# Performance work log

Measured on AMD Instinct MI355X. Metric: run time of the kernel, lower is better.

## Reference

```python
import jax, jax.numpy as jnp
import numpy as np

DIM_H = 384
EPS = 0.5
HID = 768
NN = 3   # num_normal_labels (B,I,O)
NL = 7   # num_labels (O, B/I x POS/NEG/NEU)


def _make_w_trans():
    # ote_vocab: B=0, I=1, O=2 ; ts_vocab: O=0, B-POS=1, B-NEG=2, B-NEU=3, I-POS=4, I-NEG=5, I-NEU=6
    W = np.zeros((NN, NL), dtype=np.float32)
    W[0, 1] = W[0, 2] = W[0, 3] = 1.0 / 3.0  # B -> B-*
    W[1, 4] = W[1, 5] = W[1, 6] = 1.0 / 3.0  # I -> I-*
    W[2, 0] = 1.0                            # O -> O
    return jnp.asarray(W)


def setup_inputs() -> dict:
    key = jax.random.key(0)
    ks = jax.random.split(key, 16)
    B, S = 32, 512
    s = 0.02
    inp = {
        'x': jax.random.normal(ks[0], (B, S, HID), jnp.float32),
        'attention_mask': jnp.ones((B, S), jnp.int32),
        'labels': jax.random.randint(ks[1], (B, S), 0, NL, jnp.int32),
        'labels_normal': jax.random.randint(ks[2], (B, S), 0, NN, jnp.int32),
        'W_fc_normal': jax.random.normal(ks[3], (HID, NN), jnp.float32) * s,
        'b_fc_normal': jnp.zeros((NN,), jnp.float32),
        'w_ih_f': jax.random.normal(ks[4], (4 * DIM_H, HID), jnp.float32) * s,
        'w_hh_f': jax.random.normal(ks[5], (4 * DIM_H, DIM_H), jnp.float32) * s,
        'b_f': jnp.zeros((4 * DIM_H,), jnp.float32),
        'w_ih_b': jax.random.normal(ks[6], (4 * DIM_H, HID), jnp.float32) * s,
        'w_hh_b': jax.random.normal(ks[7], (4 * DIM_H, DIM_H), jnp.float32) * s,
        'b_b': jnp.zeros((4 * DIM_H,), jnp.float32),
        'W_gate': jax.random.uniform(ks[8], (2 * DIM_H, 2 * DIM_H), jnp.float32, -0.2, 0.2),
        'W_fc_upper': jax.random.normal(ks[9], (2 * DIM_H, NL), jnp.float32) * s,
        'b_fc_upper': jnp.zeros((NL,), jnp.float32),
        'W_trans': _make_w_trans(),
    }
    return inp


def _lstm_dir(xs, w_ih, w_hh, b):
    # xs: [S, B, HID] time-major; PyTorch gate order i,f,g,o
    B = xs.shape[1]
    pre = jnp.einsum('sbh,gh->sbg', xs, w_ih) + b  # precompute input projections

    def step(carry, p_t):
        h, c = carry
        g = p_t + h @ w_hh.T
        i, f, gg, o = jnp.split(g, 4, axis=-1)
        c = jax.nn.sigmoid(f) * c + jax.nn.sigmoid(i) * jnp.tanh(gg)
        h = jax.nn.sigmoid(o) * jnp.tanh(c)
        return (h, c), h

    init = (jnp.zeros((B, DIM_H), xs.dtype), jnp.zeros((B, DIM_H), xs.dtype))
    _, hs = jax.lax.scan(step, init, pre)
    return hs  # [S, B, DIM_H]


def _masked_ce(logits, labels, mask):
    logp = jax.nn.log_softmax(logits, axis=-1)
    nll = -jnp.take_along_axis(logp, labels[..., None].astype(jnp.int32), axis=-1)[..., 0]
    m = mask.astype(logits.dtype)
    return jnp.sum(nll * m) / jnp.sum(m)


def reference(x, attention_mask, labels, labels_normal, W_fc_normal, b_fc_normal,
              w_ih_f, w_hh_f, b_f, w_ih_b, w_hh_b, b_b, W_gate,
              W_fc_upper, b_fc_upper, W_trans):
    z_t = x @ W_fc_normal + b_fc_normal                      # [B,S,NN]
    loss = _masked_ce(z_t, labels_normal, attention_mask)

    xs = jnp.transpose(x, (1, 0, 2))                         # [S,B,HID]
    hf = _lstm_dir(xs, w_ih_f, w_hh_f, b_f)
    hb = _lstm_dir(xs[::-1], w_ih_b, w_hh_b, b_b)[::-1]
    h_s = jnp.concatenate([hf, hb], axis=-1)                 # [S,B,2*DIM_H]

    # gated highway recurrence: gates depend only on h_s -> batched matmul + linear scan
    g = jax.nn.sigmoid(h_s @ W_gate)                         # [S,B,768]

    def gate_step(h_prev, inp):
        ht, gt = inp
        h = gt * ht + (1.0 - gt) * h_prev
        return h, h

    _, rest = jax.lax.scan(gate_step, h_s[0], (h_s[1:], g[1:]))
    h_tilde = jnp.concatenate([h_s[:1], rest], axis=0)       # [S,B,768]
    h_tilde = jnp.transpose(h_tilde, (1, 0, 2))              # [B,S,768]; dropout = identity (eval)

    z_s = h_tilde @ W_fc_upper + b_fc_upper                  # [B,S,NL]
    p = jax.nn.softmax(z_t, axis=-1)
    alpha = EPS * jnp.sum(p * p, axis=-1, keepdims=True)     # [B,S,1]
    z_s_prime = z_t @ W_trans                                # [B,S,NL]
    z_s_tilde = z_s_prime * alpha + z_s * (1.0 - alpha)

    loss = loss + _masked_ce(z_s_tilde, labels, attention_mask)
    return loss, z_s_tilde
```

## Files before the change

kernel.cpp:

```cpp
#include <hip/hip_runtime.h>

#define B_SZ   32
#define S_LEN  512
#define HID    768
#define DH     384
#define G4     1536
#define NPOS   16384
#define EPS_C  0.5f
#define NCH    24576
#define CHK    64
#define NCHK   8

typedef _Float16 h2 __attribute__((ext_vector_type(2)));
typedef short bf16x8 __attribute__((ext_vector_type(8)));
typedef float f32x4 __attribute__((ext_vector_type(4)));

static __device__ __forceinline__ float sigm(float x) { return 1.0f / (1.0f + __expf(-x)); }
static __device__ __forceinline__ float tanh_fast(float x) {
    return 1.0f - 2.0f / (__expf(2.0f * x) + 1.0f);
}

static __device__ __forceinline__ unsigned short f2bf(float f) {
    union { float f; unsigned u; } v; v.f = f;
    unsigned r = v.u + 0x7FFF + ((v.u >> 16) & 1);
    return (unsigned short)(r >> 16);
}
static __device__ __forceinline__ float bf2f(unsigned short u) {
    union { unsigned u; float f; } v; v.u = ((unsigned)u) << 16; return v.f;
}

static __device__ __forceinline__ float wred(float v) {
#pragma unroll
    for (int off = 32; off > 0; off >>= 1) v += __shfl_down(v, off, 64);
    return v;
}

static __device__ __forceinline__ float dot2acc(h2 a, h2 b, float c) {
#if __has_builtin(__builtin_amdgcn_fdot2)
    return __builtin_amdgcn_fdot2(a, b, c, false);
#else
    return c + (float)a.x * (float)b.x + (float)a.y * (float)b.y;
#endif
}

__global__ void wprep(const float* __restrict__ wf, const float* __restrict__ wb,
                      unsigned* __restrict__ wpk) {
    int gid = blockIdx.x * 256 + threadIdx.x;
    int d = (gid >= 294912) ? 1 : 0;
    int j = gid - d * 294912;
    const float* src = d ? wb : wf;
    _Float16 a = (_Float16)src[2 * j];
    _Float16 b = (_Float16)src[2 * j + 1];
    unsigned pa = __builtin_bit_cast(unsigned short, a);
    unsigned pb = __builtin_bit_cast(unsigned short, b);
    wpk[(size_t)d * 294912 + j] = pa | (pb << 16);
}

__global__ __launch_bounds__(256) void cast_bf16(
    const float* __restrict__ src, unsigned short* __restrict__ dst, int n4) {
    int i = blockIdx.x * 256 + threadIdx.x;
    if (i >= n4) return;
    float4 v = *(const float4*)(src + (size_t)i * 4);
    ushort4 o;
    o.x = f2bf(v.x); o.y = f2bf(v.y); o.z = f2bf(v.z); o.w = f2bf(v.w);
    *(ushort4*)(dst + (size_t)i * 4) = o;
}

__global__ __launch_bounds__(256) void wgt_prep(
    const float* __restrict__ Wg, unsigned short* __restrict__ Wgt) {
    int i = blockIdx.x * 256 + threadIdx.x;
    int k = i / 768, n = i - k * 768;
    Wgt[(size_t)n * 768 + k] = f2bf(Wg[i]);
}

__global__ __launch_bounds__(256) void zt_kernel(
    const float* __restrict__ x, const int* __restrict__ amask,
    const int* __restrict__ labn, const float* __restrict__ Wfc,
    const float* __restrict__ bfc, const float* __restrict__ Wtr,
    float* __restrict__ alpha, float* __restrict__ zsp,
    float* __restrict__ p0, float* __restrict__ p2) {
    const int gid  = blockIdx.x * blockDim.x + threadIdx.x;
    const int pos  = gid >> 6, lane = gid & 63, wv = threadIdx.x >> 6;
    __shared__ float r0[4], r2[4];
    const float* xp = x + (size_t)pos * HID;
    float a0 = 0.f, a1 = 0.f, a2 = 0.f;
#pragma unroll
    for (int j = 0; j < 12; ++j) {
        int k = lane + (j << 6);
        float xv = xp[k];
        a0 += xv * Wfc[k * 3 + 0];
        a1 += xv * Wfc[k * 3 + 1];
        a2 += xv * Wfc[k * 3 + 2];
    }
    a0 = wred(a0); a1 = wred(a1); a2 = wred(a2);
    if (lane == 0) {
        float z0 = a0 + bfc[0], z1 = a1 + bfc[1], z2 = a2 + bfc[2];
        float mx = fmaxf(z0, fmaxf(z1, z2));
        float e0 = __expf(z0 - mx), e1 = __expf(z1 - mx), e2 = __expf(z2 - mx);
        float se = e0 + e1 + e2;
        float m  = (float)amask[pos];
        int  lab = labn[pos];
        float zl = (lab == 0) ? z0 : ((lab == 1) ? z1 : z2);
        r0[wv] = (mx + __logf(se) - zl) * m;
        r2[wv] = m;
        float q0 = e0 / se, q1 = e1 / se, q2 = e2 / se;
        alpha[pos] = EPS_C * (q0 * q0 + q1 * q1 + q2 * q2);
#pragma unroll
        for (int cc = 0; cc < 7; ++cc)
            zsp[(size_t)pos * 7 + cc] = z0 * Wtr[cc] + z1 * Wtr[7 + cc] + z2 * Wtr[14 + cc];
    }
    __syncthreads();
    if (threadIdx.x == 0) {
        p0[blockIdx.x] = r0[0] + r0[1] + r0[2] + r0[3];
        p2[blockIdx.x] = r2[0] + r2[1] + r2[2] + r2[3];
    }
}

__global__ __launch_bounds__(256) void gemm_mfma(
    const unsigned short* __restrict__ A, const unsigned short* __restrict__ B,
    const float* __restrict__ bias, void* __restrict__ Cout,
    int M, int N, int K, int mode) {
    __shared__ __align__(16) unsigned short As[128][40];
    __shared__ __align__(16) unsigned short Bs[128][40];
    const int tid = threadIdx.x;
    const int m0 = blockIdx.y * 128, n0 = blockIdx.x * 128;
    const int wave = tid >> 6, lane = tid & 63;
    const int wm = (wave & 1) * 64, wn = (wave >> 1) * 64;
    const int lm = lane & 15, quad = lane >> 4;
    f32x4 acc[4][4] = {};

    for (int k0 = 0; k0 < K; k0 += 32) {
#pragma unroll
        for (int r = 0; r < 2; ++r) {
            int seg = tid + r * 256;
            int row = seg >> 2, c16 = (seg & 3) << 3;
            uint4 va = *(const uint4*)(A + (size_t)(m0 + row) * K + k0 + c16);
            *(uint4*)&As[row][c16] = va;
            uint4 vb = *(const uint4*)(B + (size_t)(n0 + row) * K + k0 + c16);
            *(uint4*)&Bs[row][c16] = vb;
        }
        __syncthreads();
        bf16x8 af[4], bfr[4];
#pragma unroll
        for (int i = 0; i < 4; ++i) {
            af[i]  = *(const bf16x8*)&As[wm + i * 16 + lm][quad * 8];
            bfr[i] = *(const bf16x8*)&Bs[wn + i * 16 + lm][quad * 8];
        }
#pragma unroll
        for (int mi = 0; mi < 4; ++mi)
#pragma unroll
            for (int ni = 0; ni < 4; ++ni)
                acc[mi][ni] = __builtin_amdgcn_mfma_f32_16x16x32_bf16(
                    af[mi], bfr[ni], acc[mi][ni], 0, 0, 0);
        __syncthreads();
    }

    const int rbase = quad * 4;
#pragma unroll
    for (int mi = 0; mi < 4; ++mi) {
#pragma unroll
        for (int ni = 0; ni < 4; ++ni) {
            const int col = n0 + wn + ni * 16 + lm;
            const float bv = (mode == 0) ? bias[col] : 0.0f;
#pragma unroll
            for (int r = 0; r < 4; ++r) {
                const int row = m0 + wm + mi * 16 + rbase + r;
                float v = acc[mi][ni][r];
                if (mode == 0)
                    ((unsigned short*)Cout)[(size_t)row * N + col] = f2bf(v + bv);
                else
                    ((float*)Cout)[(size_t)row * N + col] = sigm(v);
            }
        }
    }
}

#define WLOAD(i) const uint4 wr##i = wq[i];
#define WDOT(i) \
    a0 = dot2acc(__builtin_bit_cast(h2, wr##i.x), hp[4*(i)+0], a0); \
    a1 = dot2acc(__builtin_bit_cast(h2, wr##i.y), hp[4*(i)+1], a1); \
    a2 = dot2acc(__builtin_bit_cast(h2, wr##i.z), hp[4*(i)+2], a2); \
    a3 = dot2acc(__builtin_bit_cast(h2, wr##i.w), hp[4*(i)+3], a3);

__global__ __launch_bounds__(768) void lstm_scan3(
    const unsigned* __restrict__ wpk,
    const unsigned short* __restrict__ pre,
    unsigned short* __restrict__ h_sb,
    unsigned long long* __restrict__ hx64) {
    const int blk   = blockIdx.x;
    const int chain = blk & 63;
    const int bp    = blk >> 6;
    const int d = chain >> 5, b = chain & 31;
    const int tid = threadIdx.x;
    const int r = tid >> 1, p = tid & 1;
    const int g = r / 96;
    const int u = r - g * 96;
    const int base = bp * 96;
    const int G = g * 384 + base + u;

    __shared__ __align__(16) _Float16 lh16[384];
    __shared__ float lpre[384];

    const uint4* wq = (const uint4*)(wpk + ((size_t)d * 1536 + G) * 192 + p * 96);
    WLOAD(0)  WLOAD(1)  WLOAD(2)  WLOAD(3)  WLOAD(4)  WLOAD(5)
    WLOAD(6)  WLOAD(7)  WLOAD(8)  WLOAD(9)  WLOAD(10) WLOAD(11)
    WLOAD(12) WLOAD(13) WLOAD(14) WLOAD(15) WLOAD(16) WLOAD(17)
    WLOAD(18) WLOAD(19) WLOAD(20) WLOAD(21) WLOAD(22) WLOAD(23)

    const unsigned short* prb = pre + ((size_t)d * B_SZ + b) * S_LEN * G4;
    float c = 0.0f;

    for (int s = 0; s < S_LEN; ++s) {
        const int t = d ? (S_LEN - 1 - s) : s;
        float prev = bf2f(prb[(size_t)t * G4 + G]);

        if (s == 0) {
            if (tid < 384) lh16[tid] = (_Float16)0.0f;
        } else if (tid < 288) {
            const int uu = tid + (tid >= base ? 96 : 0);
            const unsigned long long* srcp =
                hx64 + ((size_t)((s - 1) & 1) * 64 + chain) * 384 + uu;
            unsigned long long v =
                __hip_atomic_load(srcp, __ATOMIC_RELAXED, __HIP_MEMORY_SCOPE_AGENT);
            while ((unsigned)(v >> 32) != (unsigned)(s - 1)) {
                __builtin_amdgcn_s_sleep(1);
                v = __hip_atomic_load(srcp, __ATOMIC_RELAXED, __HIP_MEMORY_SCOPE_AGENT);
            }
            lh16[uu] = (_Float16)__builtin_bit_cast(float, (unsigned)v);
        }
        __syncthreads();

        {
            const h2* hp = ((const h2*)lh16) + p * 96;
            float a0 = (p == 0) ? prev : 0.0f, a1 = 0.f, a2 = 0.f, a3 = 0.f;
            WDOT(0)  WDOT(1)  WDOT(2)  WDOT(3)  WDOT(4)  WDOT(5)
            WDOT(6)  WDOT(7)  WDOT(8)  WDOT(9)  WDOT(10) WDOT(11)
            WDOT(12) WDOT(13) WDOT(14) WDOT(15) WDOT(16) WDOT(17)
            WDOT(18) WDOT(19) WDOT(20) WDOT(21) WDOT(22) WDOT(23)
            float acc = (a0 + a1) + (a2 + a3);
            lpre[r] = acc + __shfl_xor(acc, 1, 64);
        }
        __syncthreads();

        if (tid < 96) {
            float gi = lpre[tid], gf = lpre[96 + tid], gg = lpre[192 + tid], go = lpre[288 + tid];
            c = sigm(gf) * c + sigm(gi) * tanh_fast(gg);
            float h = sigm(go) * tanh_fast(c);
            const size_t oidx = ((size_t)t * B_SZ + b) * HID + d * DH + base + tid;
            h_sb[oidx] = f2bf(h);
            lh16[base + tid] = (_Float16)h;
            unsigned long long v = ((unsigned long long)(unsigned)s << 32)
                                 | (unsigned long long)__builtin_bit_cast(unsigned, h);
            __hip_atomic_store(hx64 + ((size_t)(s & 1) * 64 + chain) * 384 + base + tid,
                               v, __ATOMIC_RELAXED, __HIP_MEMORY_SCOPE_AGENT);
        }
    }
}

__global__ __launch_bounds__(256) void gscanA(
    const float* __restrict__ g, const unsigned short* __restrict__ hsb,
    float2* __restrict__ ab) {
    int id = blockIdx.x * 256 + threadIdx.x;
    int chunk = id / NCH, chain = id - chunk * NCH;
    int t0 = chunk * CHK;
    float A = 1.f, Bv = 0.f;
    for (int i = 0; i < CHK; ++i) {
        int t = t0 + i;
        size_t idx = (size_t)t * NCH + chain;
        float gv = g[idx];
        float hv = bf2f(hsb[idx]);
        float a = (t == 0) ? 0.f : (1.f - gv);
        float bb = (t == 0) ? hv : gv * hv;
        A  = a * A;
        Bv = a * Bv + bb;
    }
    ab[id] = make_float2(A, Bv);
}

__global__ __launch_bounds__(256) void gscanB(
    const float2* __restrict__ ab, float* __restrict__ cin) {
    int chain = blockIdx.x * 256 + threadIdx.x;
    float h = 0.f;
#pragma unroll
    for (int j = 0; j < NCHK; ++j) {
        cin[(size_t)j * NCH + chain] = h;
        float2 t = ab[(size_t)j * NCH + chain];
        h = t.x * h + t.y;
    }
}

__global__ __launch_bounds__(256) void gscanC(
    const float* __restrict__ g, const unsigned short* __restrict__ hsb,
    float* __restrict__ hs, const float* __restrict__ cin) {
    int id = blockIdx.x * 256 + threadIdx.x;
    int chunk = id / NCH, chain = id - chunk * NCH;
    int t0 = chunk * CHK;
    float h = cin[(size_t)chunk * NCH + chain];
    for (int i = 0; i < CHK; ++i) {
        int t = t0 + i;
        size_t idx = (size_t)t * NCH + chain;
        float gv = g[idx];
        float v  = bf2f(hsb[idx]);
        h = (t == 0) ? v : (gv * v + (1.f - gv) * h);
        hs[idx] = h;
    }
}

__global__ __launch_bounds__(256) void final_k(
    const float* __restrict__ ht, const float* __restrict__ Wup,
    const float* __restrict__ bup, const float* __restrict__ alpha,
    const float* __restrict__ zsp, const int* __restrict__ labels,
    const int* __restrict__ amask, float* __restrict__ out, float* __restrict__ p1) {
    const int gid = blockIdx.x * blockDim.x + threadIdx.x;
    const int pos = gid >> 6, lane = gid & 63, wv = threadIdx.x >> 6;
    __shared__ float r1[4];
    const int bb = pos >> 9, tt = pos & 511;
    const float* hp = ht + (size_t)tt * (B_SZ * HID) + (size_t)bb * HID;
    float acc[7] = {};
#pragma unroll
    for (int j = 0; j < 12; ++j) {
        int k = lane + (j << 6);
        float hv = hp[k];
        const float* wr = Wup + k * 7;
#pragma unroll
        for (int cc = 0; cc < 7; ++cc) acc[cc] += hv * wr[cc];
    }
#pragma unroll
    for (int cc = 0; cc < 7; ++cc) acc[cc] = wred(acc[cc]);
    if (lane == 0) {
        float al = alpha[pos];
        float z[7], mx = -1e30f;
#pragma unroll
        for (int cc = 0; cc < 7; ++cc) {
            float v = acc[cc] + bup[cc];
            v = zsp[(size_t)pos * 7 + cc] * al + v * (1.0f - al);
            z[cc] = v;
            mx = fmaxf(mx, v);
            out[1 + (size_t)pos * 7 + cc] = v;
        }
        float se = 0.f;
#pragma unroll
        for (int cc = 0; cc < 7; ++cc) se += __expf(z[cc] - mx);
        float lse = mx + __logf(se);
        int lab = labels[pos];
        float zl = z[0];
#pragma unroll
        for (int cc = 1; cc < 7; ++cc) if (lab == cc) zl = z[cc];
        float m = (float)amask[pos];
        r1[wv] = (lse - zl) * m;
    }
    __syncthreads();
    if (threadIdx.x == 0)
        p1[blockIdx.x] = r1[0] + r1[1] + r1[2] + r1[3];
}

__global__ __launch_bounds__(256) void loss_k(
    const float* __restrict__ p0, const float* __restrict__ p1,
    const float* __restrict__ p2, float* __restrict__ out) {
    const int tid = threadIdx.x, lane = tid & 63, wv = tid >> 6;
    __shared__ float rs[4][3];
    float s0 = 0.f, s1 = 0.f, s2 = 0.f;
    for (int i = tid; i < 4096; i += 256) {
        s0 += p0[i]; s1 += p1[i]; s2 += p2[i];
    }
    s0 = wred(s0); s1 = wred(s1); s2 = wred(s2);
    if (lane == 0) { rs[wv][0] = s0; rs[wv][1] = s1; rs[wv][2] = s2; }
    __syncthreads();
    if (tid == 0) {
        float t0 = rs[0][0] + rs[1][0] + rs[2][0] + rs[3][0];
        float t1 = rs[0][1] + rs[1][1] + rs[2][1] + rs[3][1];
        float t2 = rs[0][2] + rs[1][2] + rs[2][2] + rs[3][2];
        out[0] = t0 / t2 + t1 / t2;
    }
}

extern "C" void kernel_launch(void* const* d_in, const int* in_sizes, int n_in,
                              void* d_out, int out_size, void* d_ws, size_t ws_size,
                              hipStream_t stream) {
    const float* x     = (const float*)d_in[0];
    const int*   amask = (const int*)d_in[1];
    const int*   labels= (const int*)d_in[2];
    const int*   labn  = (const int*)d_in[3];
    const float* Wfc   = (const float*)d_in[4];
    const float* bfc   = (const float*)d_in[5];
    const float* wihf  = (const float*)d_in[6];
    const float* whhf  = (const float*)d_in[7];
    const float* bf    = (const float*)d_in[8];
    const float* wihb  = (const float*)d_in[9];
    const float* whhb  = (const float*)d_in[10];
    const float* bb    = (const float*)d_in[11];
    const float* Wg    = (const float*)d_in[12];
    const float* Wup   = (const float*)d_in[13];
    const float* bup   = (const float*)d_in[14];
    const float* Wtr   = (const float*)d_in[15];
    float* out = (float*)d_out;
    (void)in_sizes; (void)n_in; (void)out_size; (void)ws_size;

    char* ws = (char*)d_ws;
    size_t off = 0;
    auto alloc = [&](size_t bytes) -> char* {
        char* p = ws + off;
        off = (off + bytes + 255) & ~(size_t)255;
        return p;
    };
    unsigned* w16buf    = (unsigned*)alloc((size_t)2 * 1536 * 192 * 4);
    unsigned short* pre = (unsigned short*)alloc((size_t)2 * NPOS * G4 * 2);
    float* hs           = (float*)alloc((size_t)NPOS * HID * 4);
    unsigned short* xb  = (unsigned short*)alloc((size_t)NPOS * HID * 2);
    unsigned short* wfb = (unsigned short*)alloc((size_t)G4 * HID * 2);
    unsigned short* wbb = (unsigned short*)alloc((size_t)G4 * HID * 2);
    unsigned short* wgt = (unsigned short*)alloc((size_t)HID * HID * 2);
    float* alpha        = (float*)alloc((size_t)NPOS * 4);
    float* zsp          = (float*)alloc((size_t)NPOS * 7 * 4);
    unsigned long long* hx64 = (unsigned long long*)alloc((size_t)2 * 64 * 384 * 8);
    float2* ab          = (float2*)alloc((size_t)NCHK * NCH * 8);
    float* cin          = (float*)alloc((size_t)NCHK * NCH * 4);
    float* part0        = (float*)alloc(4096 * 4);
    float* part1        = (float*)alloc(4096 * 4);
    float* part2        = (float*)alloc(4096 * 4);
    float* gbuf          = (float*)pre;
    unsigned short* h_sb = xb;


    wprep<<<2304, 256, 0, stream>>>(whhf, whhb, w16buf);
    cast_bf16<<<12288, 256, 0, stream>>>(x, xb, NPOS * HID / 4);
    cast_bf16<<<1152, 256, 0, stream>>>(wihf, wfb, G4 * HID / 4);
    cast_bf16<<<1152, 256, 0, stream>>>(wihb, wbb, G4 * HID / 4);
    wgt_prep<<<2304, 256, 0, stream>>>(Wg, wgt);

    zt_kernel<<<4096, 256, 0, stream>>>(x, amask, labn, Wfc, bfc, Wtr, alpha, zsp,
                                        part0, part2);

    gemm_mfma<<<dim3(12, 128), 256, 0, stream>>>(xb, wfb, bf, pre, NPOS, G4, HID, 0);
    gemm_mfma<<<dim3(12, 128), 256, 0, stream>>>(xb, wbb, bb, pre + (size_t)NPOS * G4,
                                                 NPOS, G4, HID, 0);

    lstm_scan3<<<256, 768, 0, stream>>>(w16buf, pre, h_sb, hx64);

    gemm_mfma<<<dim3(6, 128), 256, 0, stream>>>(h_sb, wgt, nullptr, gbuf, NPOS, HID, HID, 1);

    gscanA<<<768, 256, 0, stream>>>(gbuf, h_sb, ab);
    gscanB<<<96, 256, 0, stream>>>(ab, cin);
    gscanC<<<768, 256, 0, stream>>>(gbuf, h_sb, hs, cin);

    final_k<<<4096, 256, 0, stream>>>(hs, Wup, bup, alpha, zsp, labels, amask, out, part1);

    loss_k<<<1, 256, 0, stream>>>(part0, part1, part2, out);
}
```

Before: 1.291 ms.

## Remap LSTM threads so gate nonlinearity uses shuffles, dropping a block barrier

Threads are remapped so that the eight lanes covering one hidden unit (4 gates x 2 halves) sit together in a wavefront. The i/f/g/o gate sums are then gathered with warp shuffles instead of going through shared memory with a second __syncthreads. The hidden-state buffer in LDS is double-buffered so the new h can be written without racing readers. This removes one block-wide barrier per timestep of the serial recurrence. In exchange, 96 lanes spread across all waves now do the nonlinearity instead of one contiguous group, and a min-blocks-per-CU hint of 3 is added to the launch bounds.

Result: slower. 1.472 ms (+14.0%).

```diff
diff --git a/kernel.cpp b/kernel.cpp
--- a/kernel.cpp
+++ b/kernel.cpp
@@ -182,7 +182,7 @@
     a2 = dot2acc(__builtin_bit_cast(h2, wr##i.z), hp[4*(i)+2], a2); \
     a3 = dot2acc(__builtin_bit_cast(h2, wr##i.w), hp[4*(i)+3], a3);
 
-__global__ __launch_bounds__(768) void lstm_scan3(
+__global__ __launch_bounds__(768, 3) void lstm_scan4(
     const unsigned* __restrict__ wpk,
     const unsigned short* __restrict__ pre,
     unsigned short* __restrict__ h_sb,
@@ -192,14 +192,15 @@
     const int bp    = blk >> 6;
     const int d = chain >> 5, b = chain & 31;
     const int tid = threadIdx.x;
-    const int r = tid >> 1, p = tid & 1;
-    const int g = r / 96;
-    const int u = r - g * 96;
+    const int lane = tid & 63;
+    const int unit = tid >> 3;
+    const int sub  = tid & 7;
+    const int gate = sub >> 1;
+    const int p    = sub & 1;
     const int base = bp * 96;
-    const int G = g * 384 + base + u;
-
-    __shared__ __align__(16) _Float16 lh16[384];
-    __shared__ float lpre[384];
+    const int G = gate * 384 + base + unit;
+
+    __shared__ __align__(16) _Float16 lh16[2][384];
 
     const uint4* wq = (const uint4*)(wpk + ((size_t)d * 1536 + G) * 192 + p * 96);
     WLOAD(0)  WLOAD(1)  WLOAD(2)  WLOAD(3)  WLOAD(4)  WLOAD(5)
@@ -212,10 +213,11 @@
 
     for (int s = 0; s < S_LEN; ++s) {
         const int t = d ? (S_LEN - 1 - s) : s;
+        const int lb = s & 1;
         float prev = bf2f(prb[(size_t)t * G4 + G]);
 
         if (s == 0) {
-            if (tid < 384) lh16[tid] = (_Float16)0.0f;
+            if (tid < 384) lh16[0][tid] = (_Float16)0.0f;
         } else if (tid < 288) {
             const int uu = tid + (tid >= base ? 96 : 0);
             const unsigned long long* srcp =
@@ -226,32 +228,33 @@
                 __builtin_amdgcn_s_sleep(1);
                 v = __hip_atomic_load(srcp, __ATOMIC_RELAXED, __HIP_MEMORY_SCOPE_AGENT);
             }
-            lh16[uu] = (_Float16)__builtin_bit_cast(float, (unsigned)v);
+            lh16[lb][uu] = (_Float16)__builtin_bit_cast(float, (unsigned)v);
         }
         __syncthreads();
 
+        float full;
         {
-            const h2* hp = ((const h2*)lh16) + p * 96;
+            const h2* hp = ((const h2*)lh16[lb]) + p * 96;
             float a0 = (p == 0) ? prev : 0.0f, a1 = 0.f, a2 = 0.f, a3 = 0.f;
             WDOT(0)  WDOT(1)  WDOT(2)  WDOT(3)  WDOT(4)  WDOT(5)
             WDOT(6)  WDOT(7)  WDOT(8)  WDOT(9)  WDOT(10) WDOT(11)
             WDOT(12) WDOT(13) WDOT(14) WDOT(15) WDOT(16) WDOT(17)
             WDOT(18) WDOT(19) WDOT(20) WDOT(21) WDOT(22) WDOT(23)
             float acc = (a0 + a1) + (a2 + a3);
-            lpre[r] = acc + __shfl_xor(acc, 1, 64);
-        }
-        __syncthreads();
-
-        if (tid < 96) {
-            float gi = lpre[tid], gf = lpre[96 + tid], gg = lpre[192 + tid], go = lpre[288 + tid];
-            c = sigm(gf) * c + sigm(gi) * tanh_fast(gg);
+            full = acc + __shfl_xor(acc, 1, 64);
+        }
+
+        float gf = __shfl(full, lane + 2, 64);
+        float gg = __shfl(full, lane + 4, 64);
+        float go = __shfl(full, lane + 6, 64);
+        if (sub == 0) {
+            c = sigm(gf) * c + sigm(full) * tanh_fast(gg);
             float h = sigm(go) * tanh_fast(c);
-            const size_t oidx = ((size_t)t * B_SZ + b) * HID + d * DH + base + tid;
-            h_sb[oidx] = f2bf(h);
-            lh16[base + tid] = (_Float16)h;
+            h_sb[((size_t)t * B_SZ + b) * HID + d * DH + base + unit] = f2bf(h);
+            lh16[lb ^ 1][base + unit] = (_Float16)h;
             unsigned long long v = ((unsigned long long)(unsigned)s << 32)
                                  | (unsigned long long)__builtin_bit_cast(unsigned, h);
-            __hip_atomic_store(hx64 + ((size_t)(s & 1) * 64 + chain) * 384 + base + tid,
+            __hip_atomic_store(hx64 + ((size_t)lb * 64 + chain) * 384 + base + unit,
                                v, __ATOMIC_RELAXED, __HIP_MEMORY_SCOPE_AGENT);
         }
     }
@@ -435,7 +438,7 @@
     gemm_mfma<<<dim3(12, 128), 256, 0, stream>>>(xb, wbb, bb, pre + (size_t)NPOS * G4,
                                                  NPOS, G4, HID, 0);
 
-    lstm_scan3<<<256, 768, 0, stream>>>(w16buf, pre, h_sb, hx64);
+    lstm_scan4<<<256, 768, 0, stream>>>(w16buf, pre, h_sb, hx64);
 
     gemm_mfma<<<dim3(6, 128), 256, 0, stream>>>(h_sb, wgt, nullptr, gbuf, NPOS, HID, HID, 1);
 
```

## Replace second LSTM barrier with per-gate flags; store gates and highway output as bf16

Applied to the files above, without the earlier changes.

The LSTM scan double-buffers the shared hidden vector and drops the second __syncthreads. The 96 gate-combining threads now spin on per-row workgroup-scope flags, so the next step's polling can overlap the cell update. The sigmoid gate GEMM output and the highway scan result are stored as bf16, with the scan writing in place into the h_s buffer. This halves memory traffic in gscanA/C and final_k and removes the fp32 hs buffer, at the cost of precision and some spin-wait overhead in shared memory.

Result: no change. 1.271 ms (-1.5%).

```diff
diff --git a/kernel.cpp b/kernel.cpp
--- a/kernel.cpp
+++ b/kernel.cpp
@@ -169,7 +169,7 @@
                 if (mode == 0)
                     ((unsigned short*)Cout)[(size_t)row * N + col] = f2bf(v + bv);
                 else
-                    ((float*)Cout)[(size_t)row * N + col] = sigm(v);
+                    ((unsigned short*)Cout)[(size_t)row * N + col] = f2bf(sigm(v));
             }
         }
     }
@@ -182,7 +182,7 @@
     a2 = dot2acc(__builtin_bit_cast(h2, wr##i.z), hp[4*(i)+2], a2); \
     a3 = dot2acc(__builtin_bit_cast(h2, wr##i.w), hp[4*(i)+3], a3);
 
-__global__ __launch_bounds__(768) void lstm_scan3(
+__global__ __launch_bounds__(768) void lstm_scan5(
     const unsigned* __restrict__ wpk,
     const unsigned short* __restrict__ pre,
     unsigned short* __restrict__ h_sb,
@@ -198,8 +198,9 @@
     const int base = bp * 96;
     const int G = g * 384 + base + u;
 
-    __shared__ __align__(16) _Float16 lh16[384];
-    __shared__ float lpre[384];
+    __shared__ __align__(16) _Float16 lh16[2][384];
+    __shared__ float    lpreV[384];
+    __shared__ unsigned lpreT[384];
 
     const uint4* wq = (const uint4*)(wpk + ((size_t)d * 1536 + G) * 192 + p * 96);
     WLOAD(0)  WLOAD(1)  WLOAD(2)  WLOAD(3)  WLOAD(4)  WLOAD(5)
@@ -212,10 +213,11 @@
 
     for (int s = 0; s < S_LEN; ++s) {
         const int t = d ? (S_LEN - 1 - s) : s;
+        const int lb = s & 1;
         float prev = bf2f(prb[(size_t)t * G4 + G]);
 
         if (s == 0) {
-            if (tid < 384) lh16[tid] = (_Float16)0.0f;
+            if (tid < 384) { lh16[0][tid] = (_Float16)0.0f; lpreT[tid] = 0xFFFFFFFFu; }
         } else if (tid < 288) {
             const int uu = tid + (tid >= base ? 96 : 0);
             const unsigned long long* srcp =
@@ -226,39 +228,50 @@
                 __builtin_amdgcn_s_sleep(1);
                 v = __hip_atomic_load(srcp, __ATOMIC_RELAXED, __HIP_MEMORY_SCOPE_AGENT);
             }
-            lh16[uu] = (_Float16)__builtin_bit_cast(float, (unsigned)v);
+            lh16[lb][uu] = (_Float16)__builtin_bit_cast(float, (unsigned)v);
         }
         __syncthreads();
 
         {
-            const h2* hp = ((const h2*)lh16) + p * 96;
+            const h2* hp = ((const h2*)lh16[lb]) + p * 96;
             float a0 = (p == 0) ? prev : 0.0f, a1 = 0.f, a2 = 0.f, a3 = 0.f;
             WDOT(0)  WDOT(1)  WDOT(2)  WDOT(3)  WDOT(4)  WDOT(5)
             WDOT(6)  WDOT(7)  WDOT(8)  WDOT(9)  WDOT(10) WDOT(11)
             WDOT(12) WDOT(13) WDOT(14) WDOT(15) WDOT(16) WDOT(17)
             WDOT(18) WDOT(19) WDOT(20) WDOT(21) WDOT(22) WDOT(23)
             float acc = (a0 + a1) + (a2 + a3);
-            lpre[r] = acc + __shfl_xor(acc, 1, 64);
-        }
-        __syncthreads();
+            float full = acc + __shfl_xor(acc, 1, 64);
+            if (p == 0) {
+                lpreV[r] = full;
+                __hip_atomic_store(&lpreT[r], (unsigned)s, __ATOMIC_RELEASE,
+                                   __HIP_MEMORY_SCOPE_WORKGROUP);
+            }
+        }
 
         if (tid < 96) {
-            float gi = lpre[tid], gf = lpre[96 + tid], gg = lpre[192 + tid], go = lpre[288 + tid];
+            const unsigned sv = (unsigned)s;
+#pragma unroll
+            for (int j = 0; j < 4; ++j) {
+                unsigned* tp = &lpreT[j * 96 + tid];
+                while (__hip_atomic_load(tp, __ATOMIC_ACQUIRE,
+                                         __HIP_MEMORY_SCOPE_WORKGROUP) != sv) {}
+            }
+            float gi = lpreV[tid], gf = lpreV[96 + tid];
+            float gg = lpreV[192 + tid], go = lpreV[288 + tid];
             c = sigm(gf) * c + sigm(gi) * tanh_fast(gg);
             float h = sigm(go) * tanh_fast(c);
-            const size_t oidx = ((size_t)t * B_SZ + b) * HID + d * DH + base + tid;
-            h_sb[oidx] = f2bf(h);
-            lh16[base + tid] = (_Float16)h;
-            unsigned long long v = ((unsigned long long)(unsigned)s << 32)
+            unsigned long long v = ((unsigned long long)sv << 32)
                                  | (unsigned long long)__builtin_bit_cast(unsigned, h);
-            __hip_atomic_store(hx64 + ((size_t)(s & 1) * 64 + chain) * 384 + base + tid,
+            __hip_atomic_store(hx64 + ((size_t)lb * 64 + chain) * 384 + base + tid,
                                v, __ATOMIC_RELAXED, __HIP_MEMORY_SCOPE_AGENT);
+            h_sb[((size_t)t * B_SZ + b) * HID + d * DH + base + tid] = f2bf(h);
+            lh16[lb ^ 1][base + tid] = (_Float16)h;
         }
     }
 }
 
 __global__ __launch_bounds__(256) void gscanA(
-    const float* __restrict__ g, const unsigned short* __restrict__ hsb,
+    const unsigned short* __restrict__ g, const unsigned short* __restrict__ hsb,
     float2* __restrict__ ab) {
     int id = blockIdx.x * 256 + threadIdx.x;
     int chunk = id / NCH, chain = id - chunk * NCH;
@@ -267,7 +280,7 @@
     for (int i = 0; i < CHK; ++i) {
         int t = t0 + i;
         size_t idx = (size_t)t * NCH + chain;
-        float gv = g[idx];
+        float gv = bf2f(g[idx]);
         float hv = bf2f(hsb[idx]);
         float a = (t == 0) ? 0.f : (1.f - gv);
         float bb = (t == 0) ? hv : gv * hv;
@@ -290,8 +303,8 @@
 }
 
 __global__ __launch_bounds__(256) void gscanC(
-    const float* __restrict__ g, const unsigned short* __restrict__ hsb,
-    float* __restrict__ hs, const float* __restrict__ cin) {
+    const unsigned short* __restrict__ g, unsigned short* __restrict__ hsb,
+    const float* __restrict__ cin) {
     int id = blockIdx.x * 256 + threadIdx.x;
     int chunk = id / NCH, chain = id - chunk * NCH;
     int t0 = chunk * CHK;
@@ -299,15 +312,15 @@
     for (int i = 0; i < CHK; ++i) {
         int t = t0 + i;
         size_t idx = (size_t)t * NCH + chain;
-        float gv = g[idx];
+        float gv = bf2f(g[idx]);
         float v  = bf2f(hsb[idx]);
         h = (t == 0) ? v : (gv * v + (1.f - gv) * h);
-        hs[idx] = h;
+        hsb[idx] = f2bf(h);
     }
 }
 
 __global__ __launch_bounds__(256) void final_k(
-    const float* __restrict__ ht, const float* __restrict__ Wup,
+    const unsigned short* __restrict__ ht, const float* __restrict__ Wup,
     const float* __restrict__ bup, const float* __restrict__ alpha,
     const float* __restrict__ zsp, const int* __restrict__ labels,
     const int* __restrict__ amask, float* __restrict__ out, float* __restrict__ p1) {
@@ -315,12 +328,12 @@
     const int pos = gid >> 6, lane = gid & 63, wv = threadIdx.x >> 6;
     __shared__ float r1[4];
     const int bb = pos >> 9, tt = pos & 511;
-    const float* hp = ht + (size_t)tt * (B_SZ * HID) + (size_t)bb * HID;
+    const unsigned short* hp = ht + (size_t)tt * (B_SZ * HID) + (size_t)bb * HID;
     float acc[7] = {};
 #pragma unroll
     for (int j = 0; j < 12; ++j) {
         int k = lane + (j << 6);
-        float hv = hp[k];
+        float hv = bf2f(hp[k]);
         const float* wr = Wup + k * 7;
 #pragma unroll
         for (int cc = 0; cc < 7; ++cc) acc[cc] += hv * wr[cc];
@@ -405,7 +418,6 @@
     };
     unsigned* w16buf    = (unsigned*)alloc((size_t)2 * 1536 * 192 * 4);
     unsigned short* pre = (unsigned short*)alloc((size_t)2 * NPOS * G4 * 2);
-    float* hs           = (float*)alloc((size_t)NPOS * HID * 4);
     unsigned short* xb  = (unsigned short*)alloc((size_t)NPOS * HID * 2);
     unsigned short* wfb = (unsigned short*)alloc((size_t)G4 * HID * 2);
     unsigned short* wbb = (unsigned short*)alloc((size_t)G4 * HID * 2);
@@ -418,7 +430,7 @@
     float* part0        = (float*)alloc(4096 * 4);
     float* part1        = (float*)alloc(4096 * 4);
     float* part2        = (float*)alloc(4096 * 4);
-    float* gbuf          = (float*)pre;
+    unsigned short* gbuf = (unsigned short*)pre;
     unsigned short* h_sb = xb;
 
 
@@ -435,15 +447,15 @@
     gemm_mfma<<<dim3(12, 128), 256, 0, stream>>>(xb, wbb, bb, pre + (size_t)NPOS * G4,
                                                  NPOS, G4, HID, 0);
 
-    lstm_scan3<<<256, 768, 0, stream>>>(w16buf, pre, h_sb, hx64);
+    lstm_scan5<<<256, 768, 0, stream>>>(w16buf, pre, h_sb, hx64);
 
     gemm_mfma<<<dim3(6, 128), 256, 0, stream>>>(h_sb, wgt, nullptr, gbuf, NPOS, HID, HID, 1);
 
     gscanA<<<768, 256, 0, stream>>>(gbuf, h_sb, ab);
     gscanB<<<96, 256, 0, stream>>>(ab, cin);
-    gscanC<<<768, 256, 0, stream>>>(gbuf, h_sb, hs, cin);
-
-    final_k<<<4096, 256, 0, stream>>>(hs, Wup, bup, alpha, zsp, labels, amask, out, part1);
+    gscanC<<<768, 256, 0, stream>>>(gbuf, h_sb, cin);
+
+    final_k<<<4096, 256, 0, stream>>>(h_sb, Wup, bup, alpha, zsp, labels, amask, out, part1);
 
     loss_k<<<1, 256, 0, stream>>>(part0, part1, part2, out);
 }
```
